# Kernel tuning notes

Measured on AMD Instinct MI355X. Metric: run time of the kernel, lower is better.

The kernel has to match this reference:

```python
import jax, jax.numpy as jnp
import numpy as np

B, S, D = 4, 4096, 1024
GATE_THR = 0.0
ADAPT_RATIO = 0.25
MIN_K = 1
Q_MIX = 0.5
Q_WIN = 3
Q_THR = 0.5
Q_TEMP = 0.1
BUDGET_K = 2048  # ceil(0.5 * S)
CB_MIX = 0.3
CB_SIZE = 16
CB_TEMP = 0.1
CB_TOPK = 4


def setup_inputs() -> dict:
    key = jax.random.key(0)
    ks = jax.random.split(key, 6)
    x = jax.random.normal(ks[0], (B, S, D), dtype=jnp.float32)
    Wq = jax.random.normal(ks[1], (D, D), dtype=jnp.float32) * 0.02
    Wk = jax.random.normal(ks[2], (D, D), dtype=jnp.float32) * 0.02
    Wg = jax.random.normal(ks[3], (D, D), dtype=jnp.float32) * 0.02
    bg = jnp.zeros((D,), dtype=jnp.float32)
    Wm = jax.random.normal(ks[4], (D, D), dtype=jnp.float32) * 0.02
    bm = jnp.zeros((D,), dtype=jnp.float32)
    Wc = jax.random.normal(ks[5], (CB_SIZE, D), dtype=jnp.float32) * 0.02
    return {"x": x, "Wq": Wq, "Wk": Wk, "Wg": Wg, "bg": bg, "Wm": Wm, "bm": bm, "Wc": Wc}


def reference(x, Wq, Wk, Wg, bg, Wm, bm, Wc):
    # --- symplectic twist: cross-product area of consecutive (q, k) transitions ---
    q = x @ Wq.T                                 # [B,S,D]
    k = x @ Wk.T                                 # [B,S,D]
    twist = q[:, :-1] * k[:, 1:] - q[:, 1:] * k[:, :-1]   # [B,S-1,D]
    twist = jnp.pad(twist, ((0, 0), (1, 0), (0, 0)))       # pad first step -> [B,S,D]

    # --- gated SAE-style projection with adaptive top-k sparsity mask ---
    gate_pre = x @ Wg.T + bg                     # [B,S,D]
    strength = jnp.tanh(jnp.mean(jnp.abs(gate_pre), axis=-1, keepdims=True))
    kk = jnp.clip(jnp.ceil(strength * (ADAPT_RATIO * D)).astype(jnp.int32), MIN_K, D)  # [B,S,1]
    order = jnp.argsort(-gate_pre, axis=-1)      # descending rank order
    ranks = jnp.argsort(order, axis=-1)          # inverse permutation: rank of each feature
    topk_mask = ranks < kk                       # keep top-k features per token
    gate = ((gate_pre > GATE_THR) & topk_mask).astype(x.dtype)  # hard gate
    mag = jax.nn.relu(x @ Wm.T + bm)
    mu = gate * mag * twist                      # gated moment-map features [B,S,D]

    complexity = jnp.mean(jnp.abs(mu), axis=-1, keepdims=True)  # [B,S,1]

    # --- quorum consensus smoothing (avg_pool1d, count_include_pad) + budgeted top-k ---
    pad = Q_WIN // 2
    cpad = jnp.pad(complexity, ((0, 0), (pad, pad), (0, 0)))
    cs = jnp.pad(jnp.cumsum(cpad, axis=1), ((0, 0), (1, 0), (0, 0)))
    local = (cs[:, Q_WIN:] - cs[:, :-Q_WIN]) / Q_WIN            # [B,S,1] sliding mean
    quorum = jax.nn.sigmoid((local - Q_THR) / Q_TEMP)
    qr = quorum[..., 0]                                          # [B,S]
    top_idx = jax.lax.top_k(qr, BUDGET_K)[1]                     # [B,BUDGET_K]
    bmask = jnp.zeros_like(qr, dtype=bool).at[jnp.arange(B)[:, None], top_idx].set(True)
    quorum = jnp.where(bmask[..., None], quorum, 0.0)
    complexity = complexity * (1.0 - Q_MIX + Q_MIX * quorum)

    # --- codebook soft-assignment + top-k renorm + temporal shift score ---
    logits = (x @ Wc.T) / CB_TEMP                                # [B,S,CB_SIZE]
    probs = jax.nn.softmax(logits, axis=-1)
    ti = jax.lax.top_k(probs, CB_TOPK)[1]                        # [B,S,CB_TOPK]
    cmask = jnp.zeros(probs.shape, dtype=bool).at[
        jnp.arange(B)[:, None, None], jnp.arange(S)[None, :, None], ti].set(True)
    probs = jnp.where(cmask, probs, 0.0)
    probs = probs / jnp.clip(jnp.sum(probs, axis=-1, keepdims=True), 1e-8)
    shift = 0.5 * jnp.sum(jnp.abs(probs[:, 1:] - probs[:, :-1]), axis=-1, keepdims=True)
    cb_score = jnp.pad(shift, ((0, 0), (1, 0), (0, 0)))          # [B,S,1]

    complexity = (1.0 - CB_MIX) * complexity + CB_MIX * cb_score
    return complexity
```

## Files before the change

### kernel.cpp

```cpp
#include <hip/hip_runtime.h>
#include <hip/hip_bf16.h>
#include <cstdint>

#define BB 4
#define SS 4096
#define DD 1024
#define MM (BB * SS)
#define NTOT 4096
#define BUDGET 2048

typedef __attribute__((ext_vector_type(8))) short short8v;
typedef __attribute__((ext_vector_type(4))) float f32x4;

__device__ __forceinline__ float bf2f(unsigned int h) {
  return __uint_as_float(h << 16);
}
__device__ __forceinline__ unsigned short f2bf(float f) {
  unsigned int u = __float_as_uint(f);
  u = u + 0x7FFFu + ((u >> 16) & 1u);
  return (unsigned short)(u >> 16);
}
__device__ __forceinline__ unsigned int pkbf(float lo, float hi) {
  float2 f; f.x = lo; f.y = hi;
  __hip_bfloat162 h = __float22bfloat162_rn(f);
  return *(unsigned int*)&h;
}

__global__ __launch_bounds__(256) void convert_kernel(
    const float* __restrict__ x,
    const float* __restrict__ Wq, const float* __restrict__ Wk,
    const float* __restrict__ Wg, const float* __restrict__ Wm,
    unsigned short* __restrict__ xb, unsigned short* __restrict__ Wb)
{
  const size_t NX = (size_t)MM * DD;
  const size_t NCH = (NX + 4u * 1048576u) / 4;
  size_t i = (size_t)blockIdx.x * 256 + threadIdx.x;
  const size_t stride = (size_t)gridDim.x * 256;
  for (size_t c = i; c < NCH; c += stride) {
    const size_t e = c * 4;
    const float* src; unsigned short* dst;
    if (e < NX) { src = x + e; dst = xb + e; }
    else {
      const size_t w = e - NX;
      const int m = (int)(w >> 20);
      const float* Ws = (m == 0) ? Wq : (m == 1) ? Wk : (m == 2) ? Wg : Wm;
      src = Ws + (w & 1048575u); dst = Wb + w;
    }
    const float4 v = *(const float4*)src;
    uint2 o; o.x = pkbf(v.x, v.y); o.y = pkbf(v.z, v.w);
    *(uint2*)dst = o;
  }
}

__global__ __launch_bounds__(512, 2) void gemm256_kernel(
    const unsigned short* __restrict__ xb, const unsigned short* __restrict__ Wb,
    const float* __restrict__ bg, const float* __restrict__ bm,
    unsigned short* __restrict__ qb, unsigned short* __restrict__ kb,
    unsigned short* __restrict__ gb, unsigned short* __restrict__ mb)
{
  __shared__ __align__(16) unsigned short lds[32768];
  const int t  = threadIdx.x;
  const int wv = t >> 6, ln = t & 63;
  const int wr = wv >> 2, wc = wv & 3;
  const int frow = ln & 15, kc = ln >> 4;

  const int o  = blockIdx.y * 16 + blockIdx.x;
  const int L  = (o & 7) * 128 + (o >> 3);
  const int bx = L & 15, by = L >> 4;
  const int m0 = by * 256;
  const int n0 = bx * 256;
  const int mat = n0 >> 10;
  const int nc0 = n0 & 1023;

  f32x4 acc[8][4];
  #pragma unroll
  for (int i = 0; i < 8; ++i)
    #pragma unroll
    for (int j = 0; j < 4; ++j) { acc[i][j][0]=0.f; acc[i][j][1]=0.f; acc[i][j][2]=0.f; acc[i][j][3]=0.f; }

  const int srow = wv * 16 + (ln >> 2);
  const int scch = (ln & 3) << 3;
  auto stage = [&](int buf, int kt) {
    const int k0 = kt << 5;
    #pragma unroll
    for (int i = 0; i < 2; ++i) {
      const unsigned short* ga = xb + (size_t)(m0 + i * 128 + srow) * DD + k0 + scch;
      const unsigned short* gw = Wb + (size_t)(n0 + i * 128 + srow) * DD + k0 + scch;
      __builtin_amdgcn_global_load_lds(
          (const __attribute__((address_space(1))) void*)ga,
          (__attribute__((address_space(3))) void*)((__attribute__((address_space(3))) char*)lds
              + buf * 16384 + i * 8192 + wv * 1024 + ln * 16),
          16, 0, 0);
      __builtin_amdgcn_global_load_lds(
          (const __attribute__((address_space(1))) void*)gw,
          (__attribute__((address_space(3))) void*)((__attribute__((address_space(3))) char*)lds
              + 32768 + buf * 16384 + i * 8192 + wv * 1024 + ln * 16),
          16, 0, 0);
    }
  };

  stage(0, 0);
  __syncthreads();

  for (int kt = 0; kt < 32; ++kt) {
    const int cur = kt & 1;
    if (kt < 31) stage(cur ^ 1, kt + 1);

    short8v a[8], b[4];
    #pragma unroll
    for (int j = 0; j < 4; ++j)
      b[j] = *(const short8v*)&lds[16384 + cur * 8192 + (wc * 64 + j * 16 + frow) * 32 + kc * 8];
    #pragma unroll
    for (int i = 0; i < 8; ++i)
      a[i] = *(const short8v*)&lds[cur * 8192 + (wr * 128 + i * 16 + frow) * 32 + kc * 8];

    #pragma unroll
    for (int i = 0; i < 8; ++i)
      #pragma unroll
      for (int j = 0; j < 4; ++j)
        acc[i][j] = __builtin_amdgcn_mfma_f32_16x16x32_bf16(a[i], b[j], acc[i][j], 0, 0, 0);

    __syncthreads();
  }

  unsigned short* outp = (mat == 0) ? qb : (mat == 1) ? kb : (mat == 2) ? gb : mb;
  #pragma unroll
  for (int i = 0; i < 8; ++i) {
    #pragma unroll
    for (int j = 0; j < 4; ++j) {
      const int col = nc0 + wc * 64 + j * 16 + frow;
      const float bias = (mat == 2) ? bg[col] : (mat == 3) ? bm[col] : 0.f;
      #pragma unroll
      for (int r = 0; r < 4; ++r) {
        const int row = m0 + wr * 128 + i * 16 + kc * 4 + r;
        float v = acc[i][j][r] + bias;
        if (mat == 3) v = fmaxf(v, 0.0f);
        outp[(size_t)row * DD + col] = f2bf(v);
      }
    }
  }
}

__global__ __launch_bounds__(256) void mfma_gemm_fb(
    const float* __restrict__ x,
    const float* __restrict__ Wq, const float* __restrict__ Wk,
    const float* __restrict__ Wg, const float* __restrict__ Wm,
    const float* __restrict__ bg, const float* __restrict__ bm,
    unsigned short* __restrict__ q_o, unsigned short* __restrict__ k_o,
    unsigned short* __restrict__ g_o, unsigned short* __restrict__ m_o)
{
  __shared__ __align__(16) unsigned short As[128 * 32];
  __shared__ __align__(16) unsigned short Bs[128 * 32];
  const int t  = threadIdx.x;
  const int wv = t >> 6, ln = t & 63;
  const int wr = wv >> 1, wc = wv & 1;
  const int m0 = blockIdx.y * 128;
  const int n0 = blockIdx.x * 128;
  const int mat = n0 >> 10;
  const int nc0 = n0 & 1023;
  const float* __restrict__ Wsrc = (mat == 0) ? Wq : (mat == 1) ? Wk : (mat == 2) ? Wg : Wm;

  f32x4 acc[4][4];
  #pragma unroll
  for (int i = 0; i < 4; ++i)
    #pragma unroll
    for (int j = 0; j < 4; ++j) { acc[i][j][0]=0.f; acc[i][j][1]=0.f; acc[i][j][2]=0.f; acc[i][j][3]=0.f; }

  const int frow = ln & 15, kc = ln >> 4;

  for (int k0 = 0; k0 < DD; k0 += 32) {
    #pragma unroll
    for (int c = 0; c < 2; ++c) {
      const int i = c * 256 + t;
      const int row = i >> 2, colc = i & 3;
      const float* ga = x    + (size_t)(m0 + row) * DD + k0 + (colc << 3);
      const float* gw = Wsrc + (size_t)(nc0 + row) * DD + k0 + (colc << 3);
      const float4 a0 = *(const float4*)ga, a1 = *(const float4*)(ga + 4);
      const float4 b0 = *(const float4*)gw, b1 = *(const float4*)(gw + 4);
      uint4 ao, bo;
      ao.x = pkbf(a0.x, a0.y); ao.y = pkbf(a0.z, a0.w);
      ao.z = pkbf(a1.x, a1.y); ao.w = pkbf(a1.z, a1.w);
      bo.x = pkbf(b0.x, b0.y); bo.y = pkbf(b0.z, b0.w);
      bo.z = pkbf(b1.x, b1.y); bo.w = pkbf(b1.z, b1.w);
      *(uint4*)&As[row * 32 + colc * 8] = ao;
      *(uint4*)&Bs[row * 32 + colc * 8] = bo;
    }
    __syncthreads();
    short8v a[4], b[4];
    #pragma unroll
    for (int i = 0; i < 4; ++i) {
      a[i] = *(const short8v*)&As[(wr * 64 + i * 16 + frow) * 32 + kc * 8];
      b[i] = *(const short8v*)&Bs[(wc * 64 + i * 16 + frow) * 32 + kc * 8];
    }
    #pragma unroll
    for (int i = 0; i < 4; ++i)
      #pragma unroll
      for (int j = 0; j < 4; ++j)
        acc[i][j] = __builtin_amdgcn_mfma_f32_16x16x32_bf16(a[i], b[j], acc[i][j], 0, 0, 0);
    __syncthreads();
  }

  unsigned short* outp = (mat == 0) ? q_o : (mat == 1) ? k_o : (mat == 2) ? g_o : m_o;
  #pragma unroll
  for (int i = 0; i < 4; ++i) {
    #pragma unroll
    for (int j = 0; j < 4; ++j) {
      const int col = nc0 + wc * 64 + j * 16 + frow;
      #pragma unroll
      for (int r = 0; r < 4; ++r) {
        const int row = m0 + wr * 64 + i * 16 + kc * 4 + r;
        float v = acc[i][j][r];
        if (mat == 2) v += bg[col];
        if (mat == 3) v = fmaxf(v + bm[col], 0.0f);
        outp[(size_t)row * DD + col] = f2bf(v);
      }
    }
  }
}

__global__ __launch_bounds__(256) void token_kernel2(
    const float* __restrict__ x, const float* __restrict__ Wc,
    const unsigned short* __restrict__ qb, const unsigned short* __restrict__ kb,
    const unsigned short* __restrict__ gb, const unsigned short* __restrict__ mb,
    float* __restrict__ probs, float* __restrict__ craw)
{
  const int wv = threadIdx.x >> 6;
  const int ln = threadIdx.x & 63;
  const int token = blockIdx.x * 4 + wv;
  const int s = token & (SS - 1);
  const size_t rowo = (size_t)token * DD;

  const float4* x4 = (const float4*)(x + rowo);
  const float4* Wc4 = (const float4*)Wc;
  float4 xv[4];
  #pragma unroll
  for (int e = 0; e < 4; ++e) xv[e] = x4[e * 64 + ln];
  float pj[16];
  #pragma unroll
  for (int j = 0; j < 16; ++j) {
    float a = 0.f;
    #pragma unroll
    for (int e = 0; e < 4; ++e) {
      const float4 w = Wc4[j * 256 + e * 64 + ln];
      a += xv[e].x * w.x + xv[e].y * w.y + xv[e].z * w.z + xv[e].w * w.w;
    }
    pj[j] = a;
  }
  #pragma unroll
  for (int j = 0; j < 16; ++j) {
    #pragma unroll
    for (int off = 1; off < 64; off <<= 1) pj[j] += __shfl_xor(pj[j], off);
  }
  if (ln == 0) {
    float p[16];
    float mx = -3.4e38f;
    #pragma unroll
    for (int j = 0; j < 16; ++j) { p[j] = pj[j] * 10.0f; mx = fmaxf(mx, p[j]); }
    float se = 0.f;
    #pragma unroll
    for (int j = 0; j < 16; ++j) { p[j] = expf(p[j] - mx); se += p[j]; }
    const float inv = 1.0f / se;
    #pragma unroll
    for (int j = 0; j < 16; ++j) p[j] *= inv;
    unsigned int mk = 0;
    for (int it = 0; it < 4; ++it) {
      int bi = 0; float bv = -1.f;
      #pragma unroll
      for (int j = 0; j < 16; ++j)
        if (!((mk >> j) & 1u) && p[j] > bv) { bv = p[j]; bi = j; }
      mk |= 1u << bi;
    }
    float ssum = 0.f;
    #pragma unroll
    for (int j = 0; j < 16; ++j) if ((mk >> j) & 1u) ssum += p[j];
    const float rinv = 1.0f / fmaxf(ssum, 1e-8f);
    #pragma unroll
    for (int j = 0; j < 16; ++j)
      probs[(size_t)token * 16 + j] = ((mk >> j) & 1u) ? p[j] * rinv : 0.f;
  }

  if (s == 0) { if (ln == 0) craw[token] = 0.f; return; }

  unsigned short gbit[16];
  *(uint4*)&gbit[0] = *(const uint4*)(gb + rowo + ln * 16);
  *(uint4*)&gbit[8] = *(const uint4*)(gb + rowo + ln * 16 + 8);
  int ckey[16];
  float asum = 0.f;
  #pragma unroll
  for (int i = 0; i < 16; ++i) {
    const unsigned int b = gbit[i];
    ckey[i] = (b & 0x8000u) ? (int)(b ^ 0xFFFFu) : (int)(b | 0x8000u);
    asum += bf2f(b & 0x7FFFu);
  }
  #pragma unroll
  for (int off = 1; off < 64; off <<= 1) asum += __shfl_xor(asum, off);
  const float strength = tanhf(asum * (1.0f / 1024.0f));
  int kkv = (int)ceilf(strength * 256.0f);
  kkv = min(max(kkv, 1), 1024);

  int lo = 0, hi = 0xFFFF;
  while (lo < hi) {
    const int mid = (lo + hi + 1) >> 1;
    int c = 0;
    #pragma unroll
    for (int i = 0; i < 16; ++i) c += (ckey[i] >= mid);
    #pragma unroll
    for (int off = 1; off < 64; off <<= 1) c += __shfl_xor(c, off);
    if (c >= kkv) lo = mid; else hi = mid - 1;
  }
  const int T = lo;

  int cg = 0, myeq = 0;
  #pragma unroll
  for (int i = 0; i < 16; ++i) { cg += (ckey[i] > T); myeq += (ckey[i] == T); }
  #pragma unroll
  for (int off = 1; off < 64; off <<= 1) cg += __shfl_xor(cg, off);
  int incl = myeq;
  #pragma unroll
  for (int off = 1; off < 64; off <<= 1) {
    const int tt = __shfl_up(incl, off);
    if (ln >= off) incl += tt;
  }
  int ebase = incl - myeq;
  const int keep_eq = kkv - cg;

  unsigned short mB[16], qcB[16], kcB[16], qpB[16], kpB[16];
  *(uint4*)&mB[0]  = *(const uint4*)(mb + rowo + ln * 16);
  *(uint4*)&mB[8]  = *(const uint4*)(mb + rowo + ln * 16 + 8);
  *(uint4*)&qcB[0] = *(const uint4*)(qb + rowo + ln * 16);
  *(uint4*)&qcB[8] = *(const uint4*)(qb + rowo + ln * 16 + 8);
  *(uint4*)&kcB[0] = *(const uint4*)(kb + rowo + ln * 16);
  *(uint4*)&kcB[8] = *(const uint4*)(kb + rowo + ln * 16 + 8);
  *(uint4*)&qpB[0] = *(const uint4*)(qb + rowo - DD + ln * 16);
  *(uint4*)&qpB[8] = *(const uint4*)(qb + rowo - DD + ln * 16 + 8);
  *(uint4*)&kpB[0] = *(const uint4*)(kb + rowo - DD + ln * 16);
  *(uint4*)&kpB[8] = *(const uint4*)(kb + rowo - DD + ln * 16 + 8);

  float accv = 0.f;
  #pragma unroll
  for (int i = 0; i < 16; ++i) {
    const bool kp_ = (ckey[i] > T) || (ckey[i] == T && ebase < keep_eq);
    if (ckey[i] == T) ebase++;
    const unsigned int b = gbit[i];
    const bool gpos = (!(b & 0x8000u)) && (b != 0u);
    if (gpos && kp_) {
      const float tw = bf2f(qpB[i]) * bf2f(kcB[i]) - bf2f(qcB[i]) * bf2f(kpB[i]);
      accv += bf2f(mB[i]) * fabsf(tw);
    }
  }
  #pragma unroll
  for (int off = 1; off < 64; off <<= 1) accv += __shfl_xor(accv, off);
  if (ln == 0) craw[token] = accv * (1.0f / 1024.0f);
}

__global__ __launch_bounds__(256) void quorum_kernel(
    const float* __restrict__ craw, const float* __restrict__ probs,
    float* __restrict__ quorum, float* __restrict__ cb)
{
  const int idx = blockIdx.x * 256 + threadIdx.x;
  const int s = idx & (SS - 1);
  const float c1 = craw[idx];
  const float c0 = (s > 0) ? craw[idx - 1] : 0.f;
  const float c2 = (s < SS - 1) ? craw[idx + 1] : 0.f;
  const float local = (c0 + c1 + c2) / 3.0f;
  quorum[idx] = 1.0f / (1.0f + expf((0.5f - local) * 10.0f));
  float sh = 0.f;
  if (s > 0) {
    #pragma unroll
    for (int j = 0; j < 16; ++j)
      sh += fabsf(probs[(size_t)idx * 16 + j] - probs[(size_t)(idx - 1) * 16 + j]);
  }
  cb[idx] = 0.5f * sh;
}

__global__ __launch_bounds__(64) void final_kernel(
    const float* __restrict__ craw, const float* __restrict__ quorum,
    const float* __restrict__ cb, float* __restrict__ outp)
{
  const int b = blockIdx.x;
  const int ln = threadIdx.x;
  const size_t base = (size_t)b * SS;
  float qv[64]; unsigned int key[64];
  #pragma unroll
  for (int i = 0; i < 64; ++i) {
    qv[i] = quorum[base + ln * 64 + i];
    const unsigned int bb = __float_as_uint(qv[i]);
    key[i] = (bb & 0x80000000u) ? ~bb : (bb | 0x80000000u);
  }
  unsigned int lo = 0u, hi = 0xFFFFFFFFu;
  while (lo < hi) {
    const unsigned int mid = (unsigned int)(((unsigned long long)lo + hi + 1ull) >> 1);
    int c = 0;
    #pragma unroll
    for (int i = 0; i < 64; ++i) c += (key[i] >= mid);
    #pragma unroll
    for (int off = 1; off < 64; off <<= 1) c += __shfl_xor(c, off);
    if (c >= BUDGET) lo = mid; else hi = mid - 1;
  }
  const unsigned int T = lo;
  int cg = 0, myeq = 0;
  #pragma unroll
  for (int i = 0; i < 64; ++i) { cg += (key[i] > T); myeq += (key[i] == T); }
  #pragma unroll
  for (int off = 1; off < 64; off <<= 1) cg += __shfl_xor(cg, off);
  int scan = myeq;
  #pragma unroll
  for (int off = 1; off < 64; off <<= 1) {
    const int nsc = __shfl_up(scan, off);
    if (ln >= off) scan += nsc;
  }
  int ebase = scan - myeq;
  const int keep_eq = BUDGET - cg;
  #pragma unroll
  for (int i = 0; i < 64; ++i) {
    const size_t sidx = base + (size_t)ln * 64 + i;
    const bool kp_ = (key[i] > T) || (key[i] == T && ebase < keep_eq);
    if (key[i] == T) ebase++;
    const float q = kp_ ? qv[i] : 0.f;
    outp[sidx] = 0.7f * (craw[sidx] * (0.5f + 0.5f * q)) + 0.3f * cb[sidx];
  }
}

extern "C" void kernel_launch(void* const* d_in, const int* in_sizes, int n_in,
                              void* d_out, int out_size, void* d_ws, size_t ws_size,
                              hipStream_t stream)
{
  const float* x  = (const float*)d_in[0];
  const float* Wq = (const float*)d_in[1];
  const float* Wk = (const float*)d_in[2];
  const float* Wg = (const float*)d_in[3];
  const float* bg = (const float*)d_in[4];
  const float* Wm = (const float*)d_in[5];
  const float* bm = (const float*)d_in[6];
  const float* Wc = (const float*)d_in[7];
  float* outp = (float*)d_out;
  char* w = (char*)d_ws;

  const size_t SZ_BF = (size_t)MM * DD * 2;
  const size_t SMALL_OFF = 4 * SZ_BF;
  const size_t SZ_SMALL = 1048576 + 3 * 65536;

  unsigned short* qb = (unsigned short*)(w);
  unsigned short* kb = (unsigned short*)(w + SZ_BF);
  unsigned short* gb = (unsigned short*)(w + 2 * SZ_BF);
  unsigned short* mb = (unsigned short*)(w + 3 * SZ_BF);
  char* sm = w + SMALL_OFF;
  float* probs  = (float*)(sm);
  float* craw   = (float*)(sm + 1048576);
  float* quorum = (float*)(sm + 1048576 + 65536);
  float* cbuf   = (float*)(sm + 1048576 + 2 * 65536);

  const size_t need_mid = SMALL_OFF + SZ_SMALL + SZ_BF + (size_t)4 * 1048576 * 2;

  if (ws_size >= need_mid) {
    unsigned short* xb = (unsigned short*)(sm + SZ_SMALL);
    unsigned short* Wb = xb + (size_t)MM * DD;
    convert_kernel<<<2048, 256, 0, stream>>>(x, Wq, Wk, Wg, Wm, xb, Wb);
    gemm256_kernel<<<dim3(NTOT / 256, MM / 256), 512, 0, stream>>>(
        xb, Wb, bg, bm, qb, kb, gb, mb);
  } else {
    mfma_gemm_fb<<<dim3(NTOT / 128, MM / 128), 256, 0, stream>>>(
        x, Wq, Wk, Wg, Wm, bg, bm, qb, kb, gb, mb);
  }
  token_kernel2<<<dim3(MM / 4), 256, 0, stream>>>(x, Wc, qb, kb, gb, mb, probs, craw);
  quorum_kernel<<<dim3(MM / 256), 256, 0, stream>>>(craw, probs, quorum, cbuf);
  final_kernel<<<dim3(BB), 64, 0, stream>>>(craw, quorum, cbuf, outp);
}
```

Before: 296.5 us.

## Fuse codebook softmax into bf16 convert; swizzle LDS and relax GEMM barriers

The codebook logits, softmax and top-4 renormalisation move into the conversion kernel, which already reads each fp32 x row. This removes the second full read of x in the token kernel. The GEMM now XOR-swizzles its LDS layout to cut bank conflicts, and replaces __syncthreads with explicit vmcnt waits plus raw s_barrier so the next tile's loads stay in flight. The manual waitcnt scheme depends on exact counts of outstanding global-to-LDS loads, which is fragile if codegen changes.

```diff
diff --git a/kernel.cpp b/kernel.cpp
--- a/kernel.cpp
+++ b/kernel.cpp
@@ -26,29 +26,85 @@
   return *(unsigned int*)&h;
 }
 
-__global__ __launch_bounds__(256) void convert_kernel(
+__global__ __launch_bounds__(256) void convert2_kernel(
     const float* __restrict__ x,
     const float* __restrict__ Wq, const float* __restrict__ Wk,
     const float* __restrict__ Wg, const float* __restrict__ Wm,
-    unsigned short* __restrict__ xb, unsigned short* __restrict__ Wb)
-{
-  const size_t NX = (size_t)MM * DD;
-  const size_t NCH = (NX + 4u * 1048576u) / 4;
-  size_t i = (size_t)blockIdx.x * 256 + threadIdx.x;
-  const size_t stride = (size_t)gridDim.x * 256;
-  for (size_t c = i; c < NCH; c += stride) {
-    const size_t e = c * 4;
-    const float* src; unsigned short* dst;
-    if (e < NX) { src = x + e; dst = xb + e; }
-    else {
-      const size_t w = e - NX;
-      const int m = (int)(w >> 20);
-      const float* Ws = (m == 0) ? Wq : (m == 1) ? Wk : (m == 2) ? Wg : Wm;
-      src = Ws + (w & 1048575u); dst = Wb + w;
-    }
-    const float4 v = *(const float4*)src;
-    uint2 o; o.x = pkbf(v.x, v.y); o.y = pkbf(v.z, v.w);
-    *(uint2*)dst = o;
+    const float* __restrict__ Wc,
+    unsigned short* __restrict__ xb, unsigned short* __restrict__ Wb,
+    float* __restrict__ probs)
+{
+  const int blk = blockIdx.x;
+  const int t = threadIdx.x;
+  if (blk < 4096) {
+    const int wv = t >> 6, ln = t & 63;
+    const int token = blk * 4 + wv;
+    const size_t rowo = (size_t)token * DD;
+    const float4* x4 = (const float4*)(x + rowo);
+    const float4* Wc4 = (const float4*)Wc;
+    float4 xv[4];
+    #pragma unroll
+    for (int e = 0; e < 4; ++e) xv[e] = x4[e * 64 + ln];
+    uint2* xo = (uint2*)(xb + rowo);
+    #pragma unroll
+    for (int e = 0; e < 4; ++e) {
+      uint2 o; o.x = pkbf(xv[e].x, xv[e].y); o.y = pkbf(xv[e].z, xv[e].w);
+      xo[e * 64 + ln] = o;
+    }
+    float pj[16];
+    #pragma unroll
+    for (int j = 0; j < 16; ++j) {
+      float a = 0.f;
+      #pragma unroll
+      for (int e = 0; e < 4; ++e) {
+        const float4 w = Wc4[j * 256 + e * 64 + ln];
+        a += xv[e].x * w.x + xv[e].y * w.y + xv[e].z * w.z + xv[e].w * w.w;
+      }
+      pj[j] = a;
+    }
+    #pragma unroll
+    for (int j = 0; j < 16; ++j) {
+      #pragma unroll
+      for (int off = 1; off < 64; off <<= 1) pj[j] += __shfl_xor(pj[j], off);
+    }
+    if (ln == 0) {
+      float p[16];
+      float mx = -3.4e38f;
+      #pragma unroll
+      for (int j = 0; j < 16; ++j) { p[j] = pj[j] * 10.0f; mx = fmaxf(mx, p[j]); }
+      float se = 0.f;
+      #pragma unroll
+      for (int j = 0; j < 16; ++j) { p[j] = expf(p[j] - mx); se += p[j]; }
+      const float inv = 1.0f / se;
+      #pragma unroll
+      for (int j = 0; j < 16; ++j) p[j] *= inv;
+      unsigned int mk = 0;
+      for (int it = 0; it < 4; ++it) {
+        int bi = 0; float bv = -1.f;
+        #pragma unroll
+        for (int j = 0; j < 16; ++j)
+          if (!((mk >> j) & 1u) && p[j] > bv) { bv = p[j]; bi = j; }
+        mk |= 1u << bi;
+      }
+      float ssum = 0.f;
+      #pragma unroll
+      for (int j = 0; j < 16; ++j) if ((mk >> j) & 1u) ssum += p[j];
+      const float rinv = 1.0f / fmaxf(ssum, 1e-8f);
+      #pragma unroll
+      for (int j = 0; j < 16; ++j)
+        probs[(size_t)token * 16 + j] = ((mk >> j) & 1u) ? p[j] * rinv : 0.f;
+    }
+  } else {
+    const size_t off0 = (size_t)(blk - 4096) * 2048 + t * 8;
+    const int m = (int)(off0 >> 20);
+    const float* Ws = (m == 0) ? Wq : (m == 1) ? Wk : (m == 2) ? Wg : Wm;
+    const size_t wo = off0 & 1048575u;
+    const float4 a0 = *(const float4*)(Ws + wo);
+    const float4 a1 = *(const float4*)(Ws + wo + 4);
+    uint4 o;
+    o.x = pkbf(a0.x, a0.y); o.y = pkbf(a0.z, a0.w);
+    o.z = pkbf(a1.x, a1.y); o.w = pkbf(a1.z, a1.w);
+    *(uint4*)(Wb + off0) = o;
   }
 }
 
@@ -79,7 +135,7 @@
     for (int j = 0; j < 4; ++j) { acc[i][j][0]=0.f; acc[i][j][1]=0.f; acc[i][j][2]=0.f; acc[i][j][3]=0.f; }
 
   const int srow = wv * 16 + (ln >> 2);
-  const int scch = (ln & 3) << 3;
+  const int scch = (((ln & 3) ^ ((ln >> 2) & 3)) << 3);
   auto stage = [&](int buf, int kt) {
     const int k0 = kt << 5;
     #pragma unroll
@@ -100,19 +156,26 @@
   };
 
   stage(0, 0);
-  __syncthreads();
+  const int sl = ((kc ^ (frow & 3)) << 3);
 
   for (int kt = 0; kt < 32; ++kt) {
     const int cur = kt & 1;
-    if (kt < 31) stage(cur ^ 1, kt + 1);
+    if (kt < 31) {
+      stage(cur ^ 1, kt + 1);
+      asm volatile("s_waitcnt vmcnt(4)" ::: "memory");
+    } else {
+      asm volatile("s_waitcnt vmcnt(0)" ::: "memory");
+    }
+    __builtin_amdgcn_s_barrier();
+    asm volatile("" ::: "memory");
 
     short8v a[8], b[4];
     #pragma unroll
     for (int j = 0; j < 4; ++j)
-      b[j] = *(const short8v*)&lds[16384 + cur * 8192 + (wc * 64 + j * 16 + frow) * 32 + kc * 8];
+      b[j] = *(const short8v*)&lds[16384 + cur * 8192 + (wc * 64 + j * 16 + frow) * 32 + sl];
     #pragma unroll
     for (int i = 0; i < 8; ++i)
-      a[i] = *(const short8v*)&lds[cur * 8192 + (wr * 128 + i * 16 + frow) * 32 + kc * 8];
+      a[i] = *(const short8v*)&lds[cur * 8192 + (wr * 128 + i * 16 + frow) * 32 + sl];
 
     #pragma unroll
     for (int i = 0; i < 8; ++i)
@@ -120,7 +183,8 @@
       for (int j = 0; j < 4; ++j)
         acc[i][j] = __builtin_amdgcn_mfma_f32_16x16x32_bf16(a[i], b[j], acc[i][j], 0, 0, 0);
 
-    __syncthreads();
+    asm volatile("" ::: "memory");
+    __builtin_amdgcn_s_barrier();
   }
 
   unsigned short* outp = (mat == 0) ? qb : (mat == 1) ? kb : (mat == 2) ? gb : mb;
@@ -218,66 +282,16 @@
   }
 }
 
-__global__ __launch_bounds__(256) void token_kernel2(
-    const float* __restrict__ x, const float* __restrict__ Wc,
+__global__ __launch_bounds__(256) void token_kernel3(
     const unsigned short* __restrict__ qb, const unsigned short* __restrict__ kb,
     const unsigned short* __restrict__ gb, const unsigned short* __restrict__ mb,
-    float* __restrict__ probs, float* __restrict__ craw)
+    float* __restrict__ craw)
 {
   const int wv = threadIdx.x >> 6;
   const int ln = threadIdx.x & 63;
   const int token = blockIdx.x * 4 + wv;
   const int s = token & (SS - 1);
   const size_t rowo = (size_t)token * DD;
-
-  const float4* x4 = (const float4*)(x + rowo);
-  const float4* Wc4 = (const float4*)Wc;
-  float4 xv[4];
-  #pragma unroll
-  for (int e = 0; e < 4; ++e) xv[e] = x4[e * 64 + ln];
-  float pj[16];
-  #pragma unroll
-  for (int j = 0; j < 16; ++j) {
-    float a = 0.f;
-    #pragma unroll
-    for (int e = 0; e < 4; ++e) {
-      const float4 w = Wc4[j * 256 + e * 64 + ln];
-      a += xv[e].x * w.x + xv[e].y * w.y + xv[e].z * w.z + xv[e].w * w.w;
-    }
-    pj[j] = a;
-  }
-  #pragma unroll
-  for (int j = 0; j < 16; ++j) {
-    #pragma unroll
-    for (int off = 1; off < 64; off <<= 1) pj[j] += __shfl_xor(pj[j], off);
-  }
-  if (ln == 0) {
-    float p[16];
-    float mx = -3.4e38f;
-    #pragma unroll
-    for (int j = 0; j < 16; ++j) { p[j] = pj[j] * 10.0f; mx = fmaxf(mx, p[j]); }
-    float se = 0.f;
-    #pragma unroll
-    for (int j = 0; j < 16; ++j) { p[j] = expf(p[j] - mx); se += p[j]; }
-    const float inv = 1.0f / se;
-    #pragma unroll
-    for (int j = 0; j < 16; ++j) p[j] *= inv;
-    unsigned int mk = 0;
-    for (int it = 0; it < 4; ++it) {
-      int bi = 0; float bv = -1.f;
-      #pragma unroll
-      for (int j = 0; j < 16; ++j)
-        if (!((mk >> j) & 1u) && p[j] > bv) { bv = p[j]; bi = j; }
-      mk |= 1u << bi;
-    }
-    float ssum = 0.f;
-    #pragma unroll
-    for (int j = 0; j < 16; ++j) if ((mk >> j) & 1u) ssum += p[j];
-    const float rinv = 1.0f / fmaxf(ssum, 1e-8f);
-    #pragma unroll
-    for (int j = 0; j < 16; ++j)
-      probs[(size_t)token * 16 + j] = ((mk >> j) & 1u) ? p[j] * rinv : 0.f;
-  }
 
   if (s == 0) { if (ln == 0) craw[token] = 0.f; return; }
 
@@ -353,6 +367,141 @@
   if (ln == 0) craw[token] = accv * (1.0f / 1024.0f);
 }
 
+__global__ __launch_bounds__(256) void token_kernel2(
+    const float* __restrict__ x, const float* __restrict__ Wc,
+    const unsigned short* __restrict__ qb, const unsigned short* __restrict__ kb,
+    const unsigned short* __restrict__ gb, const unsigned short* __restrict__ mb,
+    float* __restrict__ probs, float* __restrict__ craw)
+{
+  const int wv = threadIdx.x >> 6;
+  const int ln = threadIdx.x & 63;
+  const int token = blockIdx.x * 4 + wv;
+  const int s = token & (SS - 1);
+  const size_t rowo = (size_t)token * DD;
+
+  const float4* x4 = (const float4*)(x + rowo);
+  const float4* Wc4 = (const float4*)Wc;
+  float4 xv[4];
+  #pragma unroll
+  for (int e = 0; e < 4; ++e) xv[e] = x4[e * 64 + ln];
+  float pj[16];
+  #pragma unroll
+  for (int j = 0; j < 16; ++j) {
+    float a = 0.f;
+    #pragma unroll
+    for (int e = 0; e < 4; ++e) {
+      const float4 w = Wc4[j * 256 + e * 64 + ln];
+      a += xv[e].x * w.x + xv[e].y * w.y + xv[e].z * w.z + xv[e].w * w.w;
+    }
+    pj[j] = a;
+  }
+  #pragma unroll
+  for (int j = 0; j < 16; ++j) {
+    #pragma unroll
+    for (int off = 1; off < 64; off <<= 1) pj[j] += __shfl_xor(pj[j], off);
+  }
+  if (ln == 0) {
+    float p[16];
+    float mx = -3.4e38f;
+    #pragma unroll
+    for (int j = 0; j < 16; ++j) { p[j] = pj[j] * 10.0f; mx = fmaxf(mx, p[j]); }
+    float se = 0.f;
+    #pragma unroll
+    for (int j = 0; j < 16; ++j) { p[j] = expf(p[j] - mx); se += p[j]; }
+    const float inv = 1.0f / se;
+    #pragma unroll
+    for (int j = 0; j < 16; ++j) p[j] *= inv;
+    unsigned int mk = 0;
+    for (int it = 0; it < 4; ++it) {
+      int bi = 0; float bv = -1.f;
+      #pragma unroll
+      for (int j = 0; j < 16; ++j)
+        if (!((mk >> j) & 1u) && p[j] > bv) { bv = p[j]; bi = j; }
+      mk |= 1u << bi;
+    }
+    float ssum = 0.f;
+    #pragma unroll
+    for (int j = 0; j < 16; ++j) if ((mk >> j) & 1u) ssum += p[j];
+    const float rinv = 1.0f / fmaxf(ssum, 1e-8f);
+    #pragma unroll
+    for (int j = 0; j < 16; ++j)
+      probs[(size_t)token * 16 + j] = ((mk >> j) & 1u) ? p[j] * rinv : 0.f;
+  }
+
+  if (s == 0) { if (ln == 0) craw[token] = 0.f; return; }
+
+  unsigned short gbit[16];
+  *(uint4*)&gbit[0] = *(const uint4*)(gb + rowo + ln * 16);
+  *(uint4*)&gbit[8] = *(const uint4*)(gb + rowo + ln * 16 + 8);
+  int ckey[16];
+  float asum = 0.f;
+  #pragma unroll
+  for (int i = 0; i < 16; ++i) {
+    const unsigned int b = gbit[i];
+    ckey[i] = (b & 0x8000u) ? (int)(b ^ 0xFFFFu) : (int)(b | 0x8000u);
+    asum += bf2f(b & 0x7FFFu);
+  }
+  #pragma unroll
+  for (int off = 1; off < 64; off <<= 1) asum += __shfl_xor(asum, off);
+  const float strength = tanhf(asum * (1.0f / 1024.0f));
+  int kkv = (int)ceilf(strength * 256.0f);
+  kkv = min(max(kkv, 1), 1024);
+
+  int lo = 0, hi = 0xFFFF;
+  while (lo < hi) {
+    const int mid = (lo + hi + 1) >> 1;
+    int c = 0;
+    #pragma unroll
+    for (int i = 0; i < 16; ++i) c += (ckey[i] >= mid);
+    #pragma unroll
+    for (int off = 1; off < 64; off <<= 1) c += __shfl_xor(c, off);
+    if (c >= kkv) lo = mid; else hi = mid - 1;
+  }
+  const int T = lo;
+
+  int cg = 0, myeq = 0;
+  #pragma unroll
+  for (int i = 0; i < 16; ++i) { cg += (ckey[i] > T); myeq += (ckey[i] == T); }
+  #pragma unroll
+  for (int off = 1; off < 64; off <<= 1) cg += __shfl_xor(cg, off);
+  int incl = myeq;
+  #pragma unroll
+  for (int off = 1; off < 64; off <<= 1) {
+    const int tt = __shfl_up(incl, off);
+    if (ln >= off) incl += tt;
+  }
+  int ebase = incl - myeq;
+  const int keep_eq = kkv - cg;
+
+  unsigned short mB[16], qcB[16], kcB[16], qpB[16], kpB[16];
+  *(uint4*)&mB[0]  = *(const uint4*)(mb + rowo + ln * 16);
+  *(uint4*)&mB[8]  = *(const uint4*)(mb + rowo + ln * 16 + 8);
+  *(uint4*)&qcB[0] = *(const uint4*)(qb + rowo + ln * 16);
+  *(uint4*)&qcB[8] = *(const uint4*)(qb + rowo + ln * 16 + 8);
+  *(uint4*)&kcB[0] = *(const uint4*)(kb + rowo + ln * 16);
+  *(uint4*)&kcB[8] = *(const uint4*)(kb + rowo + ln * 16 + 8);
+  *(uint4*)&qpB[0] = *(const uint4*)(qb + rowo - DD + ln * 16);
+  *(uint4*)&qpB[8] = *(const uint4*)(qb + rowo - DD + ln * 16 + 8);
+  *(uint4*)&kpB[0] = *(const uint4*)(kb + rowo - DD + ln * 16);
+  *(uint4*)&kpB[8] = *(const uint4*)(kb + rowo - DD + ln * 16 + 8);
+
+  float accv = 0.f;
+  #pragma unroll
+  for (int i = 0; i < 16; ++i) {
+    const bool kp_ = (ckey[i] > T) || (ckey[i] == T && ebase < keep_eq);
+    if (ckey[i] == T) ebase++;
+    const unsigned int b = gbit[i];
+    const bool gpos = (!(b & 0x8000u)) && (b != 0u);
+    if (gpos && kp_) {
+      const float tw = bf2f(qpB[i]) * bf2f(kcB[i]) - bf2f(qcB[i]) * bf2f(kpB[i]);
+      accv += bf2f(mB[i]) * fabsf(tw);
+    }
+  }
+  #pragma unroll
+  for (int off = 1; off < 64; off <<= 1) accv += __shfl_xor(accv, off);
+  if (ln == 0) craw[token] = accv * (1.0f / 1024.0f);
+}
+
 __global__ __launch_bounds__(256) void quorum_kernel(
     const float* __restrict__ craw, const float* __restrict__ probs,
     float* __restrict__ quorum, float* __restrict__ cb)
@@ -455,14 +604,16 @@
   if (ws_size >= need_mid) {
     unsigned short* xb = (unsigned short*)(sm + SZ_SMALL);
     unsigned short* Wb = xb + (size_t)MM * DD;
-    convert_kernel<<<2048, 256, 0, stream>>>(x, Wq, Wk, Wg, Wm, xb, Wb);
+    convert2_kernel<<<dim3(4096 + 2048), 256, 0, stream>>>(
+        x, Wq, Wk, Wg, Wm, Wc, xb, Wb, probs);
     gemm256_kernel<<<dim3(NTOT / 256, MM / 256), 512, 0, stream>>>(
         xb, Wb, bg, bm, qb, kb, gb, mb);
+    token_kernel3<<<dim3(MM / 4), 256, 0, stream>>>(qb, kb, gb, mb, craw);
   } else {
     mfma_gemm_fb<<<dim3(NTOT / 128, MM / 128), 256, 0, stream>>>(
         x, Wq, Wk, Wg, Wm, bg, bm, qb, kb, gb, mb);
-  }
-  token_kernel2<<<dim3(MM / 4), 256, 0, stream>>>(x, Wc, qb, kb, gb, mb, probs, craw);
+    token_kernel2<<<dim3(MM / 4), 256, 0, stream>>>(x, Wc, qb, kb, gb, mb, probs, craw);
+  }
   quorum_kernel<<<dim3(MM / 256), 256, 0, stream>>>(craw, probs, quorum, cbuf);
   final_kernel<<<dim3(BB), 64, 0, stream>>>(craw, quorum, cbuf, outp);
 }
```

After: 286.5 us. -3.4%, faster.
